# Kernel optimization log

Hardware: AMD Instinct MI355X
Metric: run time of the kernel (lower is better)

Reference implementation:

```python
import jax, jax.numpy as jnp
import numpy as np

B, S, D = 2, 2048, 2048
H, KV, HD = 16, 8, 128
THETA = 1000000.0
EPS = 1e-6


def rms_norm(x, w, eps=EPS):
    # normalize over last dim (head_dim), per Qwen3 q_norm/k_norm
    var = jnp.mean(jnp.square(x), axis=-1, keepdims=True)
    return x * jax.lax.rsqrt(var + eps) * w


def rope_cos_sin(seq_len, head_dim, theta=THETA, dtype=jnp.float32):
    inv_freq = 1.0 / (theta ** (jnp.arange(0, head_dim, 2, dtype=jnp.float32) / head_dim))
    pos = jnp.arange(seq_len, dtype=jnp.float32)
    freqs = jnp.outer(pos, inv_freq)              # [S, HD/2]
    emb = jnp.concatenate([freqs, freqs], axis=-1)  # [S, HD]
    return jnp.cos(emb).astype(dtype), jnp.sin(emb).astype(dtype)


def rotate_half(x):
    x1, x2 = jnp.split(x, 2, axis=-1)
    return jnp.concatenate([-x2, x1], axis=-1)


def setup_inputs() -> dict:
    key = jax.random.key(0)
    ks = jax.random.split(key, 8)
    sd = 1.0 / np.sqrt(D)
    return {
        "x": jax.random.normal(ks[0], (B, S, D), jnp.float32),
        "attention_mask": jnp.zeros((B, 1, S, S), jnp.float32),
        "wq": jax.random.normal(ks[1], (H * HD, D), jnp.float32) * sd,
        "wk": jax.random.normal(ks[2], (KV * HD, D), jnp.float32) * sd,
        "wv": jax.random.normal(ks[3], (KV * HD, D), jnp.float32) * sd,
        "wo": jax.random.normal(ks[4], (D, H * HD), jnp.float32) * sd,
        "q_norm_w": jnp.ones((HD,), jnp.float32),
        "k_norm_w": jnp.ones((HD,), jnp.float32),
    }


def reference(x, attention_mask, wq, wk, wv, wo, q_norm_w, k_norm_w):
    b, s, d = x.shape
    # QKV projections
    q = (x @ wq.T).reshape(b, s, H, HD)
    k = (x @ wk.T).reshape(b, s, KV, HD)
    v = (x @ wv.T).reshape(b, s, KV, HD)
    # Qwen3 per-head RMSNorm on q and k
    q = rms_norm(q, q_norm_w)
    k = rms_norm(k, k_norm_w)
    # RoPE
    cos, sin = rope_cos_sin(s, HD, dtype=x.dtype)
    cos = cos[None, :, None, :]
    sin = sin[None, :, None, :]
    q = q * cos + rotate_half(q) * sin
    k = k * cos + rotate_half(k) * sin
    # GQA: repeat kv heads to H query heads
    rep = H // KV
    k = jnp.repeat(k, rep, axis=2)  # [b, s, H, HD]
    v = jnp.repeat(v, rep, axis=2)
    # attention
    scale = 1.0 / np.sqrt(HD)
    logits = jnp.einsum("bqhd,bkhd->bhqk", q, k) * scale
    logits = logits + attention_mask
    causal = jnp.tril(jnp.ones((s, s), bool))
    logits = jnp.where(causal[None, None], logits, jnp.asarray(-1e9, logits.dtype))
    probs = jax.nn.softmax(logits, axis=-1)
    out = jnp.einsum("bhqk,bkhd->bqhd", probs, v).reshape(b, s, H * HD)
    return out @ wo.T
```

## Files before the change

kernel.cpp:

```cpp
#include <hip/hip_runtime.h>
#include <hip/hip_bf16.h>

typedef unsigned short u16;
typedef __attribute__((ext_vector_type(8))) short s16x8;
typedef __attribute__((ext_vector_type(4))) float f32x4;

#define NB 2
#define SQ 2048
#define DM 2048
#define NH 16
#define NKV 8
#define HD 128

__device__ __forceinline__ float bf2f(u16 u) {
    return __uint_as_float(((unsigned)u) << 16);
}
__device__ __forceinline__ u16 f2bf(float f) {
    unsigned u = __float_as_uint(f);
    u += 0x7FFFu + ((u >> 16) & 1u);
    return (u16)(u >> 16);
}

__device__ __forceinline__ void gload16(const void* g, void* l) {
    __builtin_amdgcn_global_load_lds((__attribute__((address_space(1))) void*)g,
                                     (__attribute__((address_space(3))) void*)l,
                                     16, 0, 0);
}

#define X4   2097152u
#define WQ4  1048576u
#define WK4   524288u
#define WV4   524288u
#define WO4  1048576u
#define P0 X4
#define P1 (P0 + WQ4)
#define P2 (P1 + WK4)
#define P3 (P2 + WV4)
#define P4 (P3 + WO4)

__global__ __launch_bounds__(256) void cvt5(const float* __restrict__ x,
                                            const float* __restrict__ wq,
                                            const float* __restrict__ wk,
                                            const float* __restrict__ wv,
                                            const float* __restrict__ wo,
                                            u16* __restrict__ xb, u16* __restrict__ wqb,
                                            u16* __restrict__ wkb, u16* __restrict__ wvb,
                                            u16* __restrict__ wob) {
    unsigned i4 = blockIdx.x * 256u + threadIdx.x;
    if (i4 >= P4) return;
    const float* src; u16* dst; unsigned off;
    if (i4 < P0)      { src = x;  dst = xb;  off = i4; }
    else if (i4 < P1) { src = wq; dst = wqb; off = i4 - P0; }
    else if (i4 < P2) { src = wk; dst = wkb; off = i4 - P1; }
    else if (i4 < P3) { src = wv; dst = wvb; off = i4 - P2; }
    else              { src = wo; dst = wob; off = i4 - P3; }
    float4 v = ((const float4*)src)[off];
    ushort4 o;
    o.x = f2bf(v.x); o.y = f2bf(v.y); o.z = f2bf(v.z); o.w = f2bf(v.w);
    ((ushort4*)dst)[off] = o;
}

__global__ __launch_bounds__(512) void gemm_qkv(const u16* __restrict__ A,
                                                const u16* __restrict__ wqb,
                                                const u16* __restrict__ wkb,
                                                const u16* __restrict__ wvb,
                                                u16* __restrict__ q_ws,
                                                u16* __restrict__ k_ws,
                                                u16* __restrict__ vt_ws) {
    __shared__ u16 SA[2][2][128 * 64];
    __shared__ u16 SB[2][2][128 * 64];
    const int K = DM;
    const int t_ = threadIdx.x;
    const int w = t_ >> 6, lane = t_ & 63;
    const int lr = lane & 15, lg = lane >> 4;
    const int m0 = blockIdx.y * 256, n0 = blockIdx.x * 256;
    const int wr = w >> 2, wc = w & 3, bh = wc >> 1;

    const u16* W; int nloc;
    if (n0 < 2048)      { W = wqb; nloc = n0; }
    else if (n0 < 3072) { W = wkb; nloc = n0 - 2048; }
    else                { W = wvb; nloc = n0 - 3072; }

    const int sr0 = t_ >> 3;
    const int sc8 = t_ & 7;

#define STG_A(hi, bufq, kk)                                                       \
    {                                                                             \
        u16* lb = &SA[bufq][hi][w * 512];                                         \
        gload16(&A[(size_t)(m0 + (hi)*128 + sr0) * K + (kk) +                     \
                   ((sc8 ^ (sr0 & 7)) * 8)], lb);                                 \
        gload16(&A[(size_t)(m0 + (hi)*128 + 64 + sr0) * K + (kk) +                \
                   ((sc8 ^ ((sr0 + 64) & 7)) * 8)], lb + 4096);                   \
    }
#define STG_B(hi, bufq, kk)                                                       \
    {                                                                             \
        u16* lb = &SB[bufq][hi][w * 512];                                         \
        gload16(&W[(size_t)(nloc + (hi)*128 + sr0) * K + (kk) +                   \
                   ((sc8 ^ (sr0 & 7)) * 8)], lb);                                 \
        gload16(&W[(size_t)(nloc + (hi)*128 + 64 + sr0) * K + (kk) +              \
                   ((sc8 ^ ((sr0 + 64) & 7)) * 8)], lb + 4096);                   \
    }

    f32x4 acc[8][4];
#pragma unroll
    for (int i = 0; i < 8; ++i)
#pragma unroll
        for (int j = 0; j < 4; ++j) acc[i][j] = (f32x4){0.f, 0.f, 0.f, 0.f};

    STG_A(0, 0, 0); STG_A(1, 0, 0); STG_B(0, 0, 0); STG_B(1, 0, 0);
    asm volatile("s_waitcnt vmcnt(0)" ::: "memory");
    __syncthreads();

    const int NT = K / 64;
    for (int t = 0; t < NT; ++t) {
        const int p = t & 1, q = p ^ 1;
        const u16* pA = &SA[p][wr][0];
        const u16* pB = &SB[p][bh][0];
        const int kk = (t + 1) * 64;
        const bool more = (t < NT - 1);

#pragma unroll
        for (int ph = 0; ph < 4; ++ph) {
            const int rh = ph >> 1, ks = ph & 1;
            if (more) {
                if (ph == 0)      STG_A(0, q, kk)
                else if (ph == 1) STG_A(1, q, kk)
                else if (ph == 2) STG_B(0, q, kk)
                else              STG_B(1, q, kk)
            }
            s16x8 af[4], bf[4];
#pragma unroll
            for (int fi = 0; fi < 4; ++fi) {
                int r = rh * 64 + fi * 16 + lr;
                af[fi] = *(const s16x8*)&pA[r * 64 + (((ks * 4 + lg) ^ (r & 7)) * 8)];
            }
#pragma unroll
            for (int fc = 0; fc < 4; ++fc) {
                int r = (wc & 1) * 64 + fc * 16 + lr;
                bf[fc] = *(const s16x8*)&pB[r * 64 + (((ks * 4 + lg) ^ (r & 7)) * 8)];
            }
            __builtin_amdgcn_s_setprio(1);
#pragma unroll
            for (int fi = 0; fi < 4; ++fi)
#pragma unroll
                for (int fc = 0; fc < 4; ++fc)
                    acc[rh * 4 + fi][fc] = __builtin_amdgcn_mfma_f32_16x16x32_bf16(
                        af[fi], bf[fc], acc[rh * 4 + fi][fc], 0, 0, 0);
            __builtin_amdgcn_s_setprio(0);
        }
        asm volatile("s_waitcnt vmcnt(0)" ::: "memory");
        __syncthreads();
    }
#undef STG_A
#undef STG_B

#pragma unroll
    for (int fr = 0; fr < 8; ++fr)
#pragma unroll
        for (int fc = 0; fc < 4; ++fc)
#pragma unroll
            for (int j = 0; j < 4; ++j) {
                int m = m0 + wr * 128 + fr * 16 + lg * 4 + j;
                int n = n0 + wc * 64 + fc * 16 + lr;
                u16 v = f2bf(acc[fr][fc][j]);
                if (n0 < 2048) {
                    q_ws[(size_t)m * 2048 + n] = v;
                } else if (n0 < 3072) {
                    k_ws[(size_t)m * 1024 + (n - 2048)] = v;
                } else {
                    int b = m >> 11, sl = m & 2047;
                    vt_ws[((size_t)b * 1024 + (n - 3072)) * 2048 + sl] = v;
                }
            }
}

__global__ __launch_bounds__(256) void gemm_out(const u16* __restrict__ A,
                                                const u16* __restrict__ W,
                                                float* __restrict__ C,
                                                int M, int N, int K) {
    __shared__ u16 Alds[128 * 32];
    __shared__ u16 Blds[128 * 32];
    const int t = threadIdx.x;
    const int w = t >> 6, lane = t & 63;
    const int lr = lane & 15, lg = lane >> 4;
    const int m0 = blockIdx.y * 128, n0 = blockIdx.x * 128;
    const int wr = w >> 1, wc = w & 1;

    f32x4 acc[4][4];
#pragma unroll
    for (int i = 0; i < 4; ++i)
#pragma unroll
        for (int j = 0; j < 4; ++j) acc[i][j] = (f32x4){0.f, 0.f, 0.f, 0.f};

    const int r_a = lane >> 2;
    const int c_a = (lane & 3) * 8;

    for (int k0 = 0; k0 < K; k0 += 32) {
#pragma unroll
        for (int s = 0; s < 2; ++s) {
            int chunk = s * 4 + w;
            int row = chunk * 16 + r_a;
            gload16(&A[(size_t)(m0 + row) * K + k0 + c_a], &Alds[chunk * 512]);
            gload16(&W[(size_t)(n0 + row) * K + k0 + c_a], &Blds[chunk * 512]);
        }
        asm volatile("s_waitcnt vmcnt(0)" ::: "memory");
        __syncthreads();

        s16x8 af[4], bfr[4];
#pragma unroll
        for (int mi = 0; mi < 4; ++mi)
            af[mi] = *(const s16x8*)&Alds[(wr * 64 + mi * 16 + lr) * 32 + lg * 8];
#pragma unroll
        for (int ni = 0; ni < 4; ++ni)
            bfr[ni] = *(const s16x8*)&Blds[(wc * 64 + ni * 16 + lr) * 32 + lg * 8];
#pragma unroll
        for (int mi = 0; mi < 4; ++mi)
#pragma unroll
            for (int ni = 0; ni < 4; ++ni)
                acc[mi][ni] = __builtin_amdgcn_mfma_f32_16x16x32_bf16(
                    af[mi], bfr[ni], acc[mi][ni], 0, 0, 0);
        __syncthreads();
    }

#pragma unroll
    for (int mi = 0; mi < 4; ++mi)
#pragma unroll
        for (int ni = 0; ni < 4; ++ni)
#pragma unroll
            for (int j = 0; j < 4; ++j) {
                int m = m0 + wr * 64 + mi * 16 + lg * 4 + j;
                int n = n0 + wc * 64 + ni * 16 + lr;
                C[(size_t)m * N + n] = acc[mi][ni][j];
            }
}

__global__ __launch_bounds__(256) void rmsrope(u16* __restrict__ qb, u16* __restrict__ kb,
                                               const float* __restrict__ qw,
                                               const float* __restrict__ kw) {
    int wid = blockIdx.x * 4 + (threadIdx.x >> 6);
    int lane = threadIdx.x & 63;
    u16* base;
    const float* w;
    int pos;
    if (wid < NB * SQ * NH) {
        int h = wid & (NH - 1), tok = wid >> 4;
        pos = tok & (SQ - 1);
        base = qb + ((size_t)tok * NH + h) * HD;
        w = qw;
    } else {
        int f = wid - NB * SQ * NH;
        int h = f & (NKV - 1), tok = f >> 3;
        pos = tok & (SQ - 1);
        base = kb + ((size_t)tok * NKV + h) * HD;
        w = kw;
    }
    float x1 = bf2f(base[lane]), x2 = bf2f(base[lane + 64]);
    float ss = x1 * x1 + x2 * x2;
#pragma unroll
    for (int off = 32; off; off >>= 1) ss += __shfl_xor(ss, off);
    float r = rsqrtf(ss * (1.f / 128.f) + 1e-6f);
    x1 *= r * w[lane];
    x2 *= r * w[lane + 64];
    float inv = exp2f((float)lane * (-19.931568569324174f / 64.f));
    float fr = (float)pos * inv;
    float c = cosf(fr);
    float sn = sinf(fr);
    base[lane]      = f2bf(x1 * c - x2 * sn);
    base[lane + 64] = f2bf(x2 * c + x1 * sn);
}

__global__ __launch_bounds__(256) void flash(const u16* __restrict__ q,
                                             const u16* __restrict__ k,
                                             const u16* __restrict__ vt,
                                             u16* __restrict__ o) {
    __shared__ u16 KB[2][64][128];
    __shared__ u16 VB[128][64];
    __shared__ u16 plds[4][16][72];
    const int bx = blockIdx.x, h = blockIdx.y, b = blockIdx.z;
    const int t = threadIdx.x;
    const int w = t >> 6, lane = t & 63;
    const int lr = lane & 15, lg = lane >> 4;
    const int kvh = h >> 1;
    const float scale = 0.08838834764831845f;

    const u16* kbase = k + (size_t)(b * SQ) * 1024 + kvh * 128;
    const u16* vbase = vt + (size_t)(b * NKV + kvh) * HD * SQ;

    for (int sidx = 0; sidx < 2; ++sidx) {
        const int qt = sidx ? (31 - bx) : bx;
        const int qrow = qt * 64 + w * 16;

        s16x8 qf[4];
        const size_t qbase = ((size_t)(b * SQ + qrow + lr) * NH + h) * HD;
#pragma unroll
        for (int ds = 0; ds < 4; ++ds)
            qf[ds] = *(const s16x8*)&q[qbase + ds * 32 + lg * 8];

        f32x4 oacc[8];
#pragma unroll
        for (int dt = 0; dt < 8; ++dt) oacc[dt] = (f32x4){0.f, 0.f, 0.f, 0.f};
        float mrow[4] = {-1e30f, -1e30f, -1e30f, -1e30f};
        float lrow[4] = {0.f, 0.f, 0.f, 0.f};

#pragma unroll
        for (int i = 0; i < 4; ++i) {
            int qq = i * 256 + t;
            int r = qq >> 4, c = qq & 15;
            gload16(kbase + (size_t)r * 1024 + (c ^ (r & 7)) * 8,
                    &KB[0][0][0] + i * 2048 + w * 512);
        }
        __syncthreads();

        int cur = 0;
        for (int kt = 0; kt <= qt; ++kt) {
            const int kv0 = kt * 64;
#pragma unroll
            for (int i = 0; i < 4; ++i) {
                int qq = i * 256 + t;
                int r = qq >> 3, c = qq & 7;
                gload16(vbase + (size_t)r * SQ + kv0 + (c ^ (r & 7)) * 8,
                        &VB[0][0] + i * 2048 + w * 512);
            }
            if (kt < qt) {
#pragma unroll
                for (int i = 0; i < 4; ++i) {
                    int qq = i * 256 + t;
                    int r = qq >> 4, c = qq & 15;
                    gload16(kbase + (size_t)(kv0 + 64 + r) * 1024 + (c ^ (r & 7)) * 8,
                            &KB[cur ^ 1][0][0] + i * 2048 + w * 512);
                }
            }

            f32x4 sc[4];
#pragma unroll
            for (int ct = 0; ct < 4; ++ct) sc[ct] = (f32x4){0.f, 0.f, 0.f, 0.f};
#pragma unroll
            for (int ds = 0; ds < 4; ++ds) {
                s16x8 kf[4];
#pragma unroll
                for (int ct = 0; ct < 4; ++ct)
                    kf[ct] = *(const s16x8*)&KB[cur][ct * 16 + lr][((ds * 4 + lg) ^ (lr & 7)) * 8];
                __builtin_amdgcn_s_setprio(1);
#pragma unroll
                for (int ct = 0; ct < 4; ++ct)
                    sc[ct] = __builtin_amdgcn_mfma_f32_16x16x32_bf16(qf[ds], kf[ct], sc[ct], 0, 0, 0);
                __builtin_amdgcn_s_setprio(0);
            }
#pragma unroll
            for (int ct = 0; ct < 4; ++ct)
#pragma unroll
                for (int j = 0; j < 4; ++j) {
                    float v = sc[ct][j] * scale;
                    if (kt == qt && (kv0 + ct * 16 + lr) > (qrow + lg * 4 + j)) v = -1e30f;
                    sc[ct][j] = v;
                }
            float mnew[4], sfac[4];
#pragma unroll
            for (int j = 0; j < 4; ++j) {
                float tm = fmaxf(fmaxf(sc[0][j], sc[1][j]), fmaxf(sc[2][j], sc[3][j]));
#pragma unroll
                for (int off = 1; off < 16; off <<= 1) tm = fmaxf(tm, __shfl_xor(tm, off));
                mnew[j] = fmaxf(mrow[j], tm);
                sfac[j] = __expf(mrow[j] - mnew[j]);
                mrow[j] = mnew[j];
            }
#pragma unroll
            for (int ct = 0; ct < 4; ++ct)
#pragma unroll
                for (int j = 0; j < 4; ++j) sc[ct][j] = __expf(sc[ct][j] - mnew[j]);
#pragma unroll
            for (int j = 0; j < 4; ++j) {
                float ssum = sc[0][j] + sc[1][j] + sc[2][j] + sc[3][j];
#pragma unroll
                for (int off = 1; off < 16; off <<= 1) ssum += __shfl_xor(ssum, off);
                lrow[j] = lrow[j] * sfac[j] + ssum;
            }
#pragma unroll
            for (int dt = 0; dt < 8; ++dt)
#pragma unroll
                for (int j = 0; j < 4; ++j) oacc[dt][j] *= sfac[j];

#pragma unroll
            for (int ct = 0; ct < 4; ++ct)
#pragma unroll
                for (int j = 0; j < 4; ++j)
                    plds[w][lg * 4 + j][ct * 16 + lr] = f2bf(sc[ct][j]);
            s16x8 pf0 = *(const s16x8*)&plds[w][lr][lg * 8];
            s16x8 pf1 = *(const s16x8*)&plds[w][lr][32 + lg * 8];

            __syncthreads();

#pragma unroll
            for (int dt = 0; dt < 8; ++dt) {
                s16x8 vf0 = *(const s16x8*)&VB[dt * 16 + lr][(lg ^ (lr & 7)) * 8];
                s16x8 vf1 = *(const s16x8*)&VB[dt * 16 + lr][((4 + lg) ^ (lr & 7)) * 8];
                __builtin_amdgcn_s_setprio(1);
                oacc[dt] = __builtin_amdgcn_mfma_f32_16x16x32_bf16(pf0, vf0, oacc[dt], 0, 0, 0);
                oacc[dt] = __builtin_amdgcn_mfma_f32_16x16x32_bf16(pf1, vf1, oacc[dt], 0, 0, 0);
                __builtin_amdgcn_s_setprio(0);
            }
            __syncthreads();
            cur ^= 1;
        }

        float inv_l[4];
#pragma unroll
        for (int j = 0; j < 4; ++j) inv_l[j] = 1.f / lrow[j];
#pragma unroll
        for (int dt = 0; dt < 8; ++dt)
#pragma unroll
            for (int j = 0; j < 4; ++j) {
                int tok = b * SQ + qrow + lg * 4 + j;
                o[((size_t)tok * NH + h) * HD + dt * 16 + lr] = f2bf(oacc[dt][j] * inv_l[j]);
            }
    }
}

extern "C" void kernel_launch(void* const* d_in, const int* in_sizes, int n_in,
                              void* d_out, int out_size, void* d_ws, size_t ws_size,
                              hipStream_t stream) {
    (void)in_sizes; (void)n_in; (void)out_size; (void)ws_size;
    const float* x   = (const float*)d_in[0];
    const float* wq  = (const float*)d_in[2];
    const float* wk  = (const float*)d_in[3];
    const float* wv  = (const float*)d_in[4];
    const float* wo  = (const float*)d_in[5];
    const float* qnw = (const float*)d_in[6];
    const float* knw = (const float*)d_in[7];

    u16* xb    = (u16*)d_ws;
    u16* q_ws  = xb    + (size_t)4096 * 2048;
    u16* k_ws  = q_ws  + (size_t)4096 * 2048;
    u16* vt_ws = k_ws  + (size_t)4096 * 1024;
    u16* wqb   = vt_ws + (size_t)4096 * 1024;
    u16* wkb   = wqb   + (size_t)2048 * 2048;
    u16* wvb   = wkb   + (size_t)1024 * 2048;
    u16* wob   = wvb   + (size_t)1024 * 2048;

    const int M = NB * SQ;

    cvt5<<<(P4 + 255) / 256, 256, 0, stream>>>(x, wq, wk, wv, wo, xb, wqb, wkb, wvb, wob);

    gemm_qkv<<<dim3(16, 16), 512, 0, stream>>>(xb, wqb, wkb, wvb, q_ws, k_ws, vt_ws);

    rmsrope<<<(NB * SQ * (NH + NKV)) / 4, 256, 0, stream>>>(q_ws, k_ws, qnw, knw);

    flash<<<dim3(16, NH, NB), 256, 0, stream>>>(q_ws, k_ws, vt_ws, q_ws);

    gemm_out<<<dim3(DM / 128, M / 128), 256, 0, stream>>>(q_ws, wob, (float*)d_out, M, DM, DM);
}
```

Baseline: 290.8 us.

## Split QKV GEMM LDS tiles into K-halves with finer-grained vmcnt pipelining

```diff
diff --git a/kernel.cpp b/kernel.cpp
--- a/kernel.cpp
+++ b/kernel.cpp
@@ -67,38 +67,37 @@
                                                 u16* __restrict__ q_ws,
                                                 u16* __restrict__ k_ws,
                                                 u16* __restrict__ vt_ws) {
-    __shared__ u16 SA[2][2][128 * 64];
-    __shared__ u16 SB[2][2][128 * 64];
+    __shared__ u16 SA[2][2][256 * 32];
+    __shared__ u16 SB[2][2][256 * 32];
     const int K = DM;
     const int t_ = threadIdx.x;
     const int w = t_ >> 6, lane = t_ & 63;
     const int lr = lane & 15, lg = lane >> 4;
     const int m0 = blockIdx.y * 256, n0 = blockIdx.x * 256;
-    const int wr = w >> 2, wc = w & 3, bh = wc >> 1;
+    const int wr = w >> 2, wc = w & 3;
 
     const u16* W; int nloc;
     if (n0 < 2048)      { W = wqb; nloc = n0; }
     else if (n0 < 3072) { W = wkb; nloc = n0 - 2048; }
     else                { W = wvb; nloc = n0 - 3072; }
 
-    const int sr0 = t_ >> 3;
-    const int sc8 = t_ & 7;
-
-#define STG_A(hi, bufq, kk)                                                       \
-    {                                                                             \
-        u16* lb = &SA[bufq][hi][w * 512];                                         \
-        gload16(&A[(size_t)(m0 + (hi)*128 + sr0) * K + (kk) +                     \
-                   ((sc8 ^ (sr0 & 7)) * 8)], lb);                                 \
-        gload16(&A[(size_t)(m0 + (hi)*128 + 64 + sr0) * K + (kk) +                \
-                   ((sc8 ^ ((sr0 + 64) & 7)) * 8)], lb + 4096);                   \
-    }
-#define STG_B(hi, bufq, kk)                                                       \
-    {                                                                             \
-        u16* lb = &SB[bufq][hi][w * 512];                                         \
-        gload16(&W[(size_t)(nloc + (hi)*128 + sr0) * K + (kk) +                   \
-                   ((sc8 ^ (sr0 & 7)) * 8)], lb);                                 \
-        gload16(&W[(size_t)(nloc + (hi)*128 + 64 + sr0) * K + (kk) +              \
-                   ((sc8 ^ ((sr0 + 64) & 7)) * 8)], lb + 4096);                   \
+    const int srow = t_ >> 2;
+    const int sc4 = t_ & 3;
+    const int schk = (sc4 ^ (srow & 3)) * 8;
+
+#define STG_A(ks, bufq, kk)                                                      \
+    {                                                                            \
+        gload16(&A[(size_t)(m0 + srow) * K + (kk) + (ks)*32 + schk],             \
+                &SA[bufq][ks][(w * 16) * 32]);                                   \
+        gload16(&A[(size_t)(m0 + 128 + srow) * K + (kk) + (ks)*32 + schk],       \
+                &SA[bufq][ks][(128 + w * 16) * 32]);                             \
+    }
+#define STG_B(ks, bufq, kk)                                                      \
+    {                                                                            \
+        gload16(&W[(size_t)(nloc + srow) * K + (kk) + (ks)*32 + schk],           \
+                &SB[bufq][ks][(w * 16) * 32]);                                   \
+        gload16(&W[(size_t)(nloc + 128 + srow) * K + (kk) + (ks)*32 + schk],     \
+                &SB[bufq][ks][(128 + w * 16) * 32]);                             \
     }
 
     f32x4 acc[8][4];
@@ -107,49 +106,81 @@
 #pragma unroll
         for (int j = 0; j < 4; ++j) acc[i][j] = (f32x4){0.f, 0.f, 0.f, 0.f};
 
-    STG_A(0, 0, 0); STG_A(1, 0, 0); STG_B(0, 0, 0); STG_B(1, 0, 0);
-    asm volatile("s_waitcnt vmcnt(0)" ::: "memory");
-    __syncthreads();
+    const int rchk = (lg ^ (lr & 3)) * 8;
+
+    STG_A(0, 0, 0); STG_B(0, 0, 0); STG_A(1, 0, 0); STG_B(1, 0, 0);
+    asm volatile("s_waitcnt vmcnt(4)\n\ts_barrier" ::: "memory");
 
     const int NT = K / 64;
     for (int t = 0; t < NT; ++t) {
-        const int p = t & 1, q = p ^ 1;
-        const u16* pA = &SA[p][wr][0];
-        const u16* pB = &SB[p][bh][0];
+        const int pb = t & 1, nbuf = pb ^ 1;
         const int kk = (t + 1) * 64;
         const bool more = (t < NT - 1);
 
-#pragma unroll
-        for (int ph = 0; ph < 4; ++ph) {
-            const int rh = ph >> 1, ks = ph & 1;
-            if (more) {
-                if (ph == 0)      STG_A(0, q, kk)
-                else if (ph == 1) STG_A(1, q, kk)
-                else if (ph == 2) STG_B(0, q, kk)
-                else              STG_B(1, q, kk)
-            }
-            s16x8 af[4], bf[4];
-#pragma unroll
-            for (int fi = 0; fi < 4; ++fi) {
-                int r = rh * 64 + fi * 16 + lr;
-                af[fi] = *(const s16x8*)&pA[r * 64 + (((ks * 4 + lg) ^ (r & 7)) * 8)];
-            }
-#pragma unroll
-            for (int fc = 0; fc < 4; ++fc) {
-                int r = (wc & 1) * 64 + fc * 16 + lr;
-                bf[fc] = *(const s16x8*)&pB[r * 64 + (((ks * 4 + lg) ^ (r & 7)) * 8)];
-            }
-            __builtin_amdgcn_s_setprio(1);
-#pragma unroll
-            for (int fi = 0; fi < 4; ++fi)
-#pragma unroll
-                for (int fc = 0; fc < 4; ++fc)
-                    acc[rh * 4 + fi][fc] = __builtin_amdgcn_mfma_f32_16x16x32_bf16(
-                        af[fi], bf[fc], acc[rh * 4 + fi][fc], 0, 0, 0);
-            __builtin_amdgcn_s_setprio(0);
-        }
-        asm volatile("s_waitcnt vmcnt(0)" ::: "memory");
-        __syncthreads();
+        s16x8 af[4], bf[4];
+
+        if (more) STG_A(0, nbuf, kk);
+#pragma unroll
+        for (int fc = 0; fc < 4; ++fc)
+            bf[fc] = *(const s16x8*)&SB[pb][0][(wc * 64 + fc * 16 + lr) * 32 + rchk];
+#pragma unroll
+        for (int fi = 0; fi < 4; ++fi)
+            af[fi] = *(const s16x8*)&SA[pb][0][(wr * 128 + fi * 16 + lr) * 32 + rchk];
+        __builtin_amdgcn_s_setprio(1);
+#pragma unroll
+        for (int fi = 0; fi < 4; ++fi)
+#pragma unroll
+            for (int fc = 0; fc < 4; ++fc)
+                acc[fi][fc] = __builtin_amdgcn_mfma_f32_16x16x32_bf16(
+                    af[fi], bf[fc], acc[fi][fc], 0, 0, 0);
+        __builtin_amdgcn_s_setprio(0);
+
+        if (more) STG_B(0, nbuf, kk);
+#pragma unroll
+        for (int fi = 0; fi < 4; ++fi)
+            af[fi] = *(const s16x8*)&SA[pb][0][(wr * 128 + 64 + fi * 16 + lr) * 32 + rchk];
+        __builtin_amdgcn_s_setprio(1);
+#pragma unroll
+        for (int fi = 0; fi < 4; ++fi)
+#pragma unroll
+            for (int fc = 0; fc < 4; ++fc)
+                acc[4 + fi][fc] = __builtin_amdgcn_mfma_f32_16x16x32_bf16(
+                    af[fi], bf[fc], acc[4 + fi][fc], 0, 0, 0);
+        __builtin_amdgcn_s_setprio(0);
+
+        if (more) asm volatile("s_waitcnt vmcnt(4)\n\ts_barrier" ::: "memory");
+        else      asm volatile("s_waitcnt vmcnt(0)\n\ts_barrier" ::: "memory");
+
+        if (more) STG_A(1, nbuf, kk);
+#pragma unroll
+        for (int fc = 0; fc < 4; ++fc)
+            bf[fc] = *(const s16x8*)&SB[pb][1][(wc * 64 + fc * 16 + lr) * 32 + rchk];
+#pragma unroll
+        for (int fi = 0; fi < 4; ++fi)
+            af[fi] = *(const s16x8*)&SA[pb][1][(wr * 128 + fi * 16 + lr) * 32 + rchk];
+        __builtin_amdgcn_s_setprio(1);
+#pragma unroll
+        for (int fi = 0; fi < 4; ++fi)
+#pragma unroll
+            for (int fc = 0; fc < 4; ++fc)
+                acc[fi][fc] = __builtin_amdgcn_mfma_f32_16x16x32_bf16(
+                    af[fi], bf[fc], acc[fi][fc], 0, 0, 0);
+        __builtin_amdgcn_s_setprio(0);
+
+        if (more) STG_B(1, nbuf, kk);
+#pragma unroll
+        for (int fi = 0; fi < 4; ++fi)
+            af[fi] = *(const s16x8*)&SA[pb][1][(wr * 128 + 64 + fi * 16 + lr) * 32 + rchk];
+        __builtin_amdgcn_s_setprio(1);
+#pragma unroll
+        for (int fi = 0; fi < 4; ++fi)
+#pragma unroll
+            for (int fc = 0; fc < 4; ++fc)
+                acc[4 + fi][fc] = __builtin_amdgcn_mfma_f32_16x16x32_bf16(
+                    af[fi], bf[fc], acc[4 + fi][fc], 0, 0, 0);
+        __builtin_amdgcn_s_setprio(0);
+
+        if (more) asm volatile("s_waitcnt vmcnt(4)\n\ts_barrier" ::: "memory");
     }
 #undef STG_A
 #undef STG_B
```

Result: faster. 284.9 us (-2.0%).
